# Kernel optimization log

Hardware: AMD Instinct MI355X
Metric: run time of the kernel (lower is better)

Reference implementation:

```python
import jax, jax.numpy as jnp
import numpy as np

B, H, W = 8, 352, 352

def _shift(x, dr, dc):
    # zero-filled shift: out[r, c] = x[r - dr, c - dc]; matches bmm with the
    # super-diagonal translation matrices in the original code.
    x = jnp.roll(x, (dr, dc), axis=(1, 2))
    if dr > 0:
        x = x.at[:, :dr, :].set(0.0)
    elif dr < 0:
        x = x.at[:, dr:, :].set(0.0)
    if dc > 0:
        x = x.at[:, :, :dc].set(0.0)
    elif dc < 0:
        x = x.at[:, :, dc:].set(0.0)
    return x

def _bilateral_vote(c):
    # c: [B, 8, H, W] sigmoid probabilities
    a1 = c[:, 3] * _shift(c[:, 4], 0, 1)    # right
    a2 = c[:, 4] * _shift(c[:, 3], 0, -1)   # left
    a3 = c[:, 1] * _shift(c[:, 6], 1, 0)    # bottom
    a4 = c[:, 6] * _shift(c[:, 1], -1, 0)   # up
    a5 = c[:, 2] * _shift(c[:, 5], 1, -1)   # left_bottom
    a6 = c[:, 5] * _shift(c[:, 2], -1, 1)   # right_above
    a7 = c[:, 0] * _shift(c[:, 7], 1, 1)    # right_bottom
    a8 = c[:, 7] * _shift(c[:, 0], -1, -1)  # left_above
    vote = jnp.stack([a7, a3, a5, a1, a2, a6, a4, a8], axis=1)
    return vote.mean(axis=1), vote  # glo_map [B,H,W], vote_out [B,8,H,W]

def _bce_sum(p, t):
    # torch F.binary_cross_entropy clamps log terms at -100
    logp = jnp.maximum(jnp.log(p), -100.0)
    log1mp = jnp.maximum(jnp.log1p(-p), -100.0)
    return -jnp.sum(t * logp + (1.0 - t) * log1mp)

def _bce2d_new(x, t):
    # weighted BCE-with-logits, sum reduction (bce2d_new in the source)
    pos = (t == 1).astype(x.dtype)
    neg = (t == 0).astype(x.dtype)
    num_pos, num_neg = pos.sum(), neg.sum()
    tot = num_pos + num_neg
    wts = (num_neg / tot) * pos + (1.1 * num_pos / tot) * neg
    ce = jnp.maximum(x, 0.0) - x * t + jnp.log1p(jnp.exp(-jnp.abs(x)))
    return jnp.sum(wts * ce)

def _forward(up_edge, up_sal, up_sal_f, target, con_target):
    con_f = con_target.astype(jnp.float32)
    sum_conn = con_f.sum(axis=1)  # [B,H,W]
    edge_map = ((sum_conn < 8) & (sum_conn > 0)).astype(jnp.float32)
    edge_l = sum(_bce2d_new(up_edge[i], edge_map[:, None]) for i in range(up_edge.shape[0]))

    def sal_term(logits):
        p = jax.nn.sigmoid(logits)
        glo, vote = _bilateral_vote(p)
        pmin = (1.0 - vote.min(axis=1)) * edge_map
        dec = glo * (1.0 - edge_map) + pmin
        dl = _bce_sum(dec[:, None], target)
        return dl + 0.2 * _bce_sum(vote, con_f) + 0.8 * _bce_sum(p, con_f)

    sal_l = sum(sal_term(up_sal[i]) for i in range(up_sal.shape[0]))
    sal_l = sal_l + sum(sal_term(up_sal_f[i]) for i in range(up_sal_f.shape[0]))
    loss = sal_l + edge_l
    return loss, edge_l, sal_l, loss

def setup_inputs() -> dict:
    key = jax.random.key(0)
    k1, k2, k3, k4, k5 = jax.random.split(key, 5)
    return {
        'up_edge': jax.random.normal(k1, (3, B, 1, H, W), jnp.float32),
        'up_sal': jax.random.normal(k2, (2, B, 8, H, W), jnp.float32),
        'up_sal_f': jax.random.normal(k3, (2, B, 8, H, W), jnp.float32),
        'target': jax.random.uniform(k4, (B, 1, H, W), jnp.float32),
        'con_target': jax.random.randint(k5, (B, 8, H, W), 0, 2, jnp.int32),
        'edge': 0, 'weight': 1, 'voted': 0, 'unbalance': 0,
    }

def reference(up_edge, up_sal, up_sal_f, target, con_target, edge, weight, voted, unbalance):
    # edge is overwritten inside forward; weight/voted/unbalance are unused.
    return _forward(up_edge, up_sal, up_sal_f, target, con_target)
```

## Files before the change

kernel.cpp:

```cpp
#include <hip/hip_runtime.h>
#include <math.h>

#define HH 352
#define WW 352
#define IMG (HH * WW)
#define NPIX (8 * IMG)
#define NG (NPIX / 4)
#define IMG4 (IMG / 4)
#define WB (WW / 4)
#define THREADS 256
#define GBLK (NG / THREADS)

typedef float f4 __attribute__((ext_vector_type(4)));
typedef int   i4 __attribute__((ext_vector_type(4)));

__device__ __forceinline__ float rcpf_(float x) { return __builtin_amdgcn_rcpf(x); }

__device__ __forceinline__ f4 loadu4(const float* p) {
    f4 v;
    __builtin_memcpy(&v, p, 16);
    return v;
}

__device__ __forceinline__ float wave_reduce_f(float v) {
    #pragma unroll
    for (int off = 32; off > 0; off >>= 1) v += __shfl_down(v, off, 64);
    return v;
}
__device__ __forceinline__ int wave_reduce_i(int v) {
    #pragma unroll
    for (int off = 32; off > 0; off >>= 1) v += __shfl_down(v, off, 64);
    return v;
}

__device__ __forceinline__ void block_acc(float v, double* dst) {
    v = wave_reduce_f(v);
    __shared__ float sm[4];
    int lane = threadIdx.x & 63, wid = threadIdx.x >> 6;
    if (lane == 0) sm[wid] = v;
    __syncthreads();
    if (threadIdx.x == 0)
        atomicAdd(dst, (double)(sm[0] + sm[1] + sm[2] + sm[3]));
}

__global__ __launch_bounds__(THREADS, 4) void k_main(
        const float* __restrict__ up_edge,
        const float* __restrict__ up_sal,
        const float* __restrict__ up_sal_f,
        const float* __restrict__ target,
        const int* __restrict__ con,
        double* __restrict__ acc,
        unsigned int* __restrict__ npos) {
    int g = blockIdx.x * THREADS + threadIdx.x;
    int y = blockIdx.y;
    int b = g / IMG4;
    int r4 = g - b * IMG4;

    const int* cb = con + (size_t)b * 8 * IMG + 4 * (size_t)r4;
    i4 c[8];
    #pragma unroll
    for (int k = 0; k < 8; k++) c[k] = *(const i4*)(cb + (size_t)k * IMG);

    unsigned int byte_[4];
    float em_[4];
    #pragma unroll
    for (int j = 0; j < 4; j++) {
        unsigned int by = 0; int s = 0;
        #pragma unroll
        for (int k = 0; k < 8; k++) { int cv = c[k][j]; s += cv; by |= ((unsigned)cv) << k; }
        byte_[j] = by;
        em_[j] = (s > 0 && s < 8) ? 1.0f : 0.0f;
    }

    if (y == 0) {
        f4 x[3];
        #pragma unroll
        for (int i = 0; i < 3; i++)
            x[i] = *(const f4*)(up_edge + (size_t)i * NPIX + 4 * (size_t)g);
        float sp = 0.0f, sn = 0.0f; int cnt = 0;
        #pragma unroll
        for (int j = 0; j < 4; j++) {
            float em = em_[j], ce = 0.0f;
            #pragma unroll
            for (int i = 0; i < 3; i++) {
                float xx = x[i][j];
                ce += fmaxf(xx, 0.0f) - xx * em + __logf(1.0f + __expf(-fabsf(xx)));
            }
            sp += em * ce;
            sn += (1.0f - em) * ce;
            cnt += (int)em;
        }
        sp = wave_reduce_f(sp);
        sn = wave_reduce_f(sn);
        cnt = wave_reduce_i(cnt);
        __shared__ float smp[4], smn[4];
        __shared__ int smc[4];
        int lane = threadIdx.x & 63, wid = threadIdx.x >> 6;
        if (lane == 0) { smp[wid] = sp; smn[wid] = sn; smc[wid] = cnt; }
        __syncthreads();
        if (threadIdx.x == 0) {
            atomicAdd(acc + 0, (double)(smp[0] + smp[1] + smp[2] + smp[3]));
            atomicAdd(acc + 1, (double)(smn[0] + smn[1] + smn[2] + smn[3]));
            atomicAdd(npos, (unsigned int)(smc[0] + smc[1] + smc[2] + smc[3]));
        }
        return;
    }

    int s4 = y - 1;
    int h  = r4 / WB;
    int wb = r4 - h * WB;
    const float* tb = (s4 < 2) ? (up_sal + (size_t)s4 * 8 * NPIX)
                               : (up_sal_f + (size_t)(s4 - 2) * 8 * NPIX);
    const float* base = tb + (size_t)b * 8 * IMG;

    f4 tgt = *(const f4*)(target + 4 * (size_t)g);

    const int drs[8] = {-1, -1, -1,  0, 0,  1, 1, 1};
    const int dcs[8] = {-1,  0,  1, -1, 1, -1, 0, 1};

    f4 xc[8], xn[8];
    float hok[8];
    #pragma unroll
    for (int k = 0; k < 8; k++) {
        xc[k] = *(const f4*)(base + (size_t)k * IMG + 4 * (size_t)r4);
        int h2 = h + drs[k];
        long off = (long)(7 - k) * IMG + (long)h2 * WW + 4 * wb + dcs[k];
        off = off < 0 ? 0 : off;
        off = off > (long)(8 * IMG - 4) ? (long)(8 * IMG - 4) : off;
        xn[k] = loadu4(base + off);
        hok[k] = ((unsigned)h2 < (unsigned)HH) ? 1.0f : 0.0f;
    }

    float local = 0.0f;
    #pragma unroll
    for (int j = 0; j < 4; j++) {
        unsigned int byte = byte_[j];
        float em = em_[j];
        float vsum = 0.0f, vmin = 1e30f, vb = 0.0f, pb = 0.0f;
        #pragma unroll
        for (int k = 0; k < 8; k++) {
            float okc = hok[k];
            if (dcs[k] == -1 && j == 0) okc = (wb != 0)      ? okc : 0.0f;
            if (dcs[k] ==  1 && j == 3) okc = (wb != WB - 1) ? okc : 0.0f;

            float xcv = xc[k][j];
            float e   = __expf(-xcv);
            float pc  = rcpf_(1.0f + e);
            float sc  = __logf(1.0f + e);
            float en  = __expf(-xn[k][j]);
            float pn  = rcpf_(1.0f + en) * okc;

            float v = pc * pn;
            vsum += v;
            vmin = fminf(vmin, v);

            bool t = (byte >> k) & 1u;
            float arg = t ? v : (1.0f - v);
            vb += fminf(-__logf(arg), 100.0f);
            float pbk = t ? sc : (xcv + sc);
            pb += fminf(pbk, 100.0f);
        }
        float glo = vsum * 0.125f;
        float dec = (em != 0.0f) ? (1.0f - vmin) : glo;
        float lgd  = fmaxf(__logf(dec), -100.0f);
        float lg1d = fmaxf(__logf(1.0f - dec), -100.0f);
        local += -(tgt[j] * lgd + (1.0f - tgt[j]) * lg1d) + 0.2f * vb + 0.8f * pb;
    }
    block_acc(local, acc + 2);
}

__global__ void k_final(const double* __restrict__ acc,
                        const unsigned int* __restrict__ npos,
                        float* __restrict__ out) {
    if (threadIdx.x == 0) {
        double np_  = (double)(*npos);
        double tot  = (double)NPIX;
        double nn   = tot - np_;
        double wpos = nn / tot;
        double wneg = 1.1 * np_ / tot;
        double e  = wpos * acc[0] + wneg * acc[1];
        double sl = acc[2];
        double l  = e + sl;
        out[0] = (float)l;
        out[1] = (float)e;
        out[2] = (float)sl;
        out[3] = (float)l;
    }
}

extern "C" void kernel_launch(void* const* d_in, const int* in_sizes, int n_in,
                              void* d_out, int out_size, void* d_ws, size_t ws_size,
                              hipStream_t stream) {
    const float* up_edge  = (const float*)d_in[0];
    const float* up_sal   = (const float*)d_in[1];
    const float* up_sal_f = (const float*)d_in[2];
    const float* target   = (const float*)d_in[3];
    const int*   con      = (const int*)d_in[4];
    float* out = (float*)d_out;

    double*       acc  = (double*)d_ws;
    unsigned int* npos = (unsigned int*)((char*)d_ws + 24);

    hipMemsetAsync(d_ws, 0, 64, stream);
    k_main<<<dim3(GBLK, 5), THREADS, 0, stream>>>(up_edge, up_sal, up_sal_f,
                                                  target, con, acc, npos);
    k_final<<<1, 64, 0, stream>>>(acc, npos, out);
}
```

Baseline: 240.1 us.

## Pre-pack connectivity targets into bitmasks and simplify neighbor offset math

Adds a pre-pass kernel that packs the 8 int32 connectivity channels into one byte per pixel, four pixels to a 32-bit word. The main kernel then reads one word per thread instead of 128 bytes of int data in each of its five y-slices, and derives the edge mask from the byte. Neighbor offsets are also computed with 32-bit ints and clamped rows. The trade-off is an extra launch plus a full read of the int tensor and a write of the packed buffer to the workspace.

```diff
diff --git a/kernel.cpp b/kernel.cpp
--- a/kernel.cpp
+++ b/kernel.cpp
@@ -43,12 +43,30 @@
         atomicAdd(dst, (double)(sm[0] + sm[1] + sm[2] + sm[3]));
 }
 
+__global__ void k_pack(const int* __restrict__ con,
+                       unsigned int* __restrict__ packed) {
+    int g = blockIdx.x * THREADS + threadIdx.x;
+    int b = g / IMG4;
+    int r4 = g - b * IMG4;
+    const int* cb = con + (size_t)b * 8 * IMG + 4 * (size_t)r4;
+    unsigned int pk = 0;
+    #pragma unroll
+    for (int k = 0; k < 8; k++) {
+        i4 c = *(const i4*)(cb + (size_t)k * IMG);
+        pk |= ((unsigned)c[0]) << k;
+        pk |= ((unsigned)c[1]) << (8 + k);
+        pk |= ((unsigned)c[2]) << (16 + k);
+        pk |= ((unsigned)c[3]) << (24 + k);
+    }
+    packed[g] = pk;
+}
+
 __global__ __launch_bounds__(THREADS, 4) void k_main(
         const float* __restrict__ up_edge,
         const float* __restrict__ up_sal,
         const float* __restrict__ up_sal_f,
         const float* __restrict__ target,
-        const int* __restrict__ con,
+        const unsigned int* __restrict__ packed,
         double* __restrict__ acc,
         unsigned int* __restrict__ npos) {
     int g = blockIdx.x * THREADS + threadIdx.x;
@@ -56,20 +74,14 @@
     int b = g / IMG4;
     int r4 = g - b * IMG4;
 
-    const int* cb = con + (size_t)b * 8 * IMG + 4 * (size_t)r4;
-    i4 c[8];
-    #pragma unroll
-    for (int k = 0; k < 8; k++) c[k] = *(const i4*)(cb + (size_t)k * IMG);
-
+    unsigned int pk = packed[g];
     unsigned int byte_[4];
     float em_[4];
     #pragma unroll
     for (int j = 0; j < 4; j++) {
-        unsigned int by = 0; int s = 0;
-        #pragma unroll
-        for (int k = 0; k < 8; k++) { int cv = c[k][j]; s += cv; by |= ((unsigned)cv) << k; }
+        unsigned int by = (pk >> (8 * j)) & 0xffu;
         byte_[j] = by;
-        em_[j] = (s > 0 && s < 8) ? 1.0f : 0.0f;
+        em_[j] = (by != 0u && by != 0xffu) ? 1.0f : 0.0f;
     }
 
     if (y == 0) {
@@ -109,6 +121,7 @@
     int s4 = y - 1;
     int h  = r4 / WB;
     int wb = r4 - h * WB;
+    int ro = 4 * r4 - h * WW;
     const float* tb = (s4 < 2) ? (up_sal + (size_t)s4 * 8 * NPIX)
                                : (up_sal_f + (size_t)(s4 - 2) * 8 * NPIX);
     const float* base = tb + (size_t)b * 8 * IMG;
@@ -122,11 +135,12 @@
     float hok[8];
     #pragma unroll
     for (int k = 0; k < 8; k++) {
-        xc[k] = *(const f4*)(base + (size_t)k * IMG + 4 * (size_t)r4);
-        int h2 = h + drs[k];
-        long off = (long)(7 - k) * IMG + (long)h2 * WW + 4 * wb + dcs[k];
-        off = off < 0 ? 0 : off;
-        off = off > (long)(8 * IMG - 4) ? (long)(8 * IMG - 4) : off;
+        xc[k] = *(const f4*)(base + k * IMG + 4 * r4);
+        int h2  = h + drs[k];
+        int h2c = min(max(h2, 0), HH - 1);
+        int off = (7 - k) * IMG + h2c * WW + ro + dcs[k];
+        off = max(off, 0);
+        off = min(off, 8 * IMG - 4);
         xn[k] = loadu4(base + off);
         hok[k] = ((unsigned)h2 < (unsigned)HH) ? 1.0f : 0.0f;
     }
@@ -198,11 +212,13 @@
     const int*   con      = (const int*)d_in[4];
     float* out = (float*)d_out;
 
-    double*       acc  = (double*)d_ws;
-    unsigned int* npos = (unsigned int*)((char*)d_ws + 24);
+    double*       acc    = (double*)d_ws;
+    unsigned int* npos   = (unsigned int*)((char*)d_ws + 24);
+    unsigned int* packed = (unsigned int*)((char*)d_ws + 64);
 
     hipMemsetAsync(d_ws, 0, 64, stream);
+    k_pack<<<GBLK, THREADS, 0, stream>>>(con, packed);
     k_main<<<dim3(GBLK, 5), THREADS, 0, stream>>>(up_edge, up_sal, up_sal_f,
-                                                  target, con, acc, npos);
+                                                  target, packed, acc, npos);
     k_final<<<1, 64, 0, stream>>>(acc, npos, out);
 }
```

New measurement: 239.2 us. No clear change (-0.4%).
